# Kernel optimization log

Hardware: AMD Instinct MI355X
Metric: run time of the kernel (lower is better)

## Reference

```python
import jax, jax.numpy as jnp
import numpy as np

EPS = 1e-5
SLOPE = 0.01  # LeakyReLU default negative_slope
D_STATE = 16


def leaky(x):
    return jnp.where(x >= 0, x, SLOPE * x)


def instance_norm(x):
    # InstanceNorm3d(affine=False): normalize per (n, c) over spatial dims
    m = x.mean(axis=(2, 3, 4), keepdims=True)
    v = x.var(axis=(2, 3, 4), keepdims=True)
    return (x - m) * jax.lax.rsqrt(v + EPS)


def conv3d(x, w, b, groups=1, pad=0):
    y = jax.lax.conv_general_dilated(
        x, w, (1, 1, 1), [(pad, pad)] * 3,
        dimension_numbers=('NCDHW', 'OIDHW', 'NCDHW'),
        feature_group_count=groups)
    return y + b[None, :, None, None, None]


def conv_transpose2(x, w, b):
    # ConvTranspose3d(k=2, s=2): non-overlapping, so it is a pure einsum+interleave
    # x: [n,c,d,h,w], w: [c,o,2,2,2] (torch layout)
    y = jnp.einsum('ncdhw,coijk->nodihjwk', x, w)
    n, o, d, _, h, _, ww, _ = y.shape
    return y.reshape(n, o, 2 * d, 2 * h, 2 * ww) + b[None, :, None, None, None]


def selective_scan(u, dt, A, B, C, D):
    # u, dt: [b,l,d]; A: [d,n]; B, C: [b,l,n]; D: [d]
    dA = jnp.exp(dt[..., None] * A)                              # [b,l,d,n]
    dBu = dt[..., None] * B[:, :, None, :] * u[..., None]        # [b,l,d,n]

    def step(h, inp):
        dA_t, dBu_t, C_t = inp
        h = dA_t * h + dBu_t                                     # [b,d,n]
        y = jnp.einsum('bdn,bn->bd', h, C_t)
        return h, y

    h0 = jnp.zeros((u.shape[0],) + A.shape, u.dtype)
    _, ys = jax.lax.scan(
        step, h0,
        (dA.transpose(1, 0, 2, 3), dBu.transpose(1, 0, 2, 3), C.transpose(1, 0, 2)))
    return ys.transpose(1, 0, 2) + u * D                         # [b,l,d]


def mamba_block(x, in_proj_w, conv1d_w, conv1d_b, x_proj_w,
                dt_proj_w, dt_proj_b, A_log, D_param, out_proj_w):
    # x: [b,l,c]
    dt_rank = dt_proj_w.shape[1]
    xz = x @ in_proj_w.T                                         # [b,l,2*d_inner]
    xi, z = jnp.split(xz, 2, axis=-1)
    # causal depthwise conv1d over sequence (torch pads d_conv-1 both sides, keeps [:L])
    xi_c = xi.transpose(0, 2, 1)                                 # [b,d_inner,l]
    xi_c = jax.lax.conv_general_dilated(
        xi_c, conv1d_w, (1,), [(conv1d_w.shape[-1] - 1, 0)],
        dimension_numbers=('NCH', 'OIH', 'NCH'),
        feature_group_count=xi_c.shape[1])
    xi = jax.nn.silu(xi_c + conv1d_b[None, :, None]).transpose(0, 2, 1)  # [b,l,d_inner]
    x_dbl = xi @ x_proj_w.T
    dt, B, C = jnp.split(x_dbl, [dt_rank, dt_rank + D_STATE], axis=-1)
    dt = jax.nn.softplus(dt @ dt_proj_w.T + dt_proj_b)
    A = -jnp.exp(A_log)
    y = selective_scan(xi, dt, A, B, C, D_param)
    y = y * jax.nn.silu(z)
    return y @ out_proj_w.T


def layer_norm(x, w, b):
    m = x.mean(-1, keepdims=True)
    v = x.var(-1, keepdims=True)
    return (x - m) * jax.lax.rsqrt(v + EPS) * w + b


def up_forward(x1, x2, up_w, up_b, dc1_w, dc1_b, dc2_w, dc2_b, dc3_w, dc3_b,
               ln_w, ln_b, in_proj_w, conv1d_w, conv1d_b, x_proj_w,
               dt_proj_w, dt_proj_b, A_log, D_param, out_proj_w):
    x1 = conv_transpose2(x1, up_w, up_b)
    dZ = x2.shape[2] - x1.shape[2]
    dY = x2.shape[3] - x1.shape[3]
    dX = x2.shape[4] - x1.shape[4]
    x1 = jnp.pad(x1, ((0, 0), (0, 0),
                      (dZ // 2, dZ - dZ // 2),
                      (dY // 2, dY - dY // 2),
                      (dX // 2, dX - dX // 2)))
    x = jnp.concatenate([x2, x1], axis=1)
    # DoubleConv (residual=False since in_channels != out_channels)
    x = leaky(instance_norm(conv3d(x, dc1_w, dc1_b)))
    x = leaky(instance_norm(conv3d(x, dc2_w, dc2_b, groups=8, pad=1)))
    x = leaky(instance_norm(conv3d(x, dc3_w, dc3_b)))
    # MambaLayer over flattened spatial tokens
    b, c, d, h, w = x.shape
    t = x.transpose(0, 2, 3, 4, 1).reshape(b, d * h * w, c)
    t = layer_norm(t, ln_w, ln_b)
    t = mamba_block(t, in_proj_w, conv1d_w, conv1d_b, x_proj_w,
                    dt_proj_w, dt_proj_b, A_log, D_param, out_proj_w)
    return t.reshape(b, d, h, w, c).transpose(0, 4, 1, 2, 3)


def setup_inputs() -> dict:
    key = jax.random.key(0)
    ks = jax.random.split(key, 20)
    c_out = 32      # out_channels / d_model
    d_inner = 64    # expand * d_model
    dt_rank = 2     # ceil(32/16)
    s = 0.02
    return {
        'x1': jax.random.normal(ks[0], (2, 32, 8, 16, 16), jnp.float32),
        'x2': jax.random.normal(ks[1], (2, 32, 16, 32, 32), jnp.float32),
        'up_w': jax.random.normal(ks[2], (32, 32, 2, 2, 2), jnp.float32) * s,
        'up_b': jnp.zeros((32,), jnp.float32),
        'dc1_w': jax.random.normal(ks[3], (32, 64, 1, 1, 1), jnp.float32) * s,
        'dc1_b': jnp.zeros((32,), jnp.float32),
        'dc2_w': jax.random.normal(ks[4], (32, 4, 3, 3, 3), jnp.float32) * s,
        'dc2_b': jnp.zeros((32,), jnp.float32),
        'dc3_w': jax.random.normal(ks[5], (32, 32, 1, 1, 1), jnp.float32) * s,
        'dc3_b': jnp.zeros((32,), jnp.float32),
        'ln_w': jnp.ones((c_out,), jnp.float32),
        'ln_b': jnp.zeros((c_out,), jnp.float32),
        'in_proj_w': jax.random.normal(ks[6], (2 * d_inner, c_out), jnp.float32) * s,
        'conv1d_w': jax.random.normal(ks[7], (d_inner, 1, 4), jnp.float32) * s,
        'conv1d_b': jnp.zeros((d_inner,), jnp.float32),
        'x_proj_w': jax.random.normal(ks[8], (dt_rank + 2 * D_STATE, d_inner), jnp.float32) * s,
        'dt_proj_w': jax.random.normal(ks[9], (d_inner, dt_rank), jnp.float32) * s,
        'dt_proj_b': jnp.full((d_inner,), -4.0, jnp.float32),
        'A_log': jnp.log(jnp.tile(jnp.arange(1.0, D_STATE + 1.0, dtype=jnp.float32), (d_inner, 1))),
        'D_param': jnp.ones((d_inner,), jnp.float32),
        'out_proj_w': jax.random.normal(ks[10], (c_out, d_inner), jnp.float32) * s,
    }


def reference(x1, x2, up_w, up_b, dc1_w, dc1_b, dc2_w, dc2_b, dc3_w, dc3_b,
              ln_w, ln_b, in_proj_w, conv1d_w, conv1d_b, x_proj_w,
              dt_proj_w, dt_proj_b, A_log, D_param, out_proj_w):
    return up_forward(x1, x2, up_w, up_b, dc1_w, dc1_b, dc2_w, dc2_b, dc3_w, dc3_b,
                      ln_w, ln_b, in_proj_w, conv1d_w, conv1d_b, x_proj_w,
                      dt_proj_w, dt_proj_b, A_log, D_param, out_proj_w)
```

## Files before the change

kernel.cpp:

```cpp
#include <hip/hip_runtime.h>

#define TPB 256
#define S_TOT 16384
#define NCHUNK 512
#define CLEN 32
#define EPS 1e-5f
#define SLOPE 0.01f

__device__ __forceinline__ float leakyf(float v){ return v > 0.f ? v : SLOPE * v; }
__device__ __forceinline__ float siluf(float v){ return v / (1.f + __expf(-v)); }

__global__ __launch_bounds__(TPB) void k_upc1(
    const float* __restrict__ x1, const float* __restrict__ x2,
    const float* __restrict__ upw, const float* __restrict__ upb,
    const float* __restrict__ w1, const float* __restrict__ b1,
    float* __restrict__ c1, float* st1p) {
  __shared__ float wq[8192];
  __shared__ float sup[64*33];
  __shared__ float red[4][8][2];
  int t = threadIdx.x, bid = blockIdx.x;
  int sb = bid & 255, n = bid >> 8;
  int p = t & 63, os = t >> 6;
  int s = sb*64 + p;
  for (int i = t; i < 8192; i += TPB) wq[i] = upw[i];
  __syncthreads();
  int z = s >> 10, y = (s >> 5) & 31, x = s & 31;
  int tap = ((z & 1)*2 + (y & 1))*2 + (x & 1);
  int xb = n*65536 + (z >> 1)*256 + (y >> 1)*16 + (x >> 1);
  float xv[32];
  #pragma unroll
  for (int c = 0; c < 32; c++) xv[c] = x1[xb + c*2048];
  float up[8];
  #pragma unroll
  for (int j = 0; j < 8; j++) up[j] = upb[os*8 + j];
  #pragma unroll
  for (int c = 0; c < 32; c++) {
    #pragma unroll
    for (int j = 0; j < 8; j++)
      up[j] += xv[c] * wq[c*256 + (os*8 + j)*8 + tap];
  }
  #pragma unroll
  for (int j = 0; j < 8; j++) sup[p*33 + os*8 + j] = up[j];
  __syncthreads();
  int c0 = os*8;
  float acc[8];
  #pragma unroll
  for (int j = 0; j < 8; j++) acc[j] = b1[c0 + j];
  const float* px2 = x2 + n*32*S_TOT + s;
  #pragma unroll
  for (int i = 0; i < 32; i++) {
    float v = px2[i*S_TOT];
    #pragma unroll
    for (int j = 0; j < 8; j++) acc[j] += v * w1[(c0 + j)*64 + i];
  }
  #pragma unroll
  for (int o = 0; o < 32; o++) {
    float v = sup[p*33 + o];
    #pragma unroll
    for (int j = 0; j < 8; j++) acc[j] += v * w1[(c0 + j)*64 + 32 + o];
  }
  #pragma unroll
  for (int j = 0; j < 8; j++)
    c1[(n*32 + c0 + j)*S_TOT + s] = acc[j];
  int wv = t >> 6;
  #pragma unroll
  for (int j = 0; j < 8; j++) {
    float sm = acc[j], sq = acc[j]*acc[j];
    #pragma unroll
    for (int o = 32; o > 0; o >>= 1) { sm += __shfl_down(sm, o); sq += __shfl_down(sq, o); }
    if ((t & 63) == 0) { red[wv][j][0] = sm; red[wv][j][1] = sq; }
  }
  __syncthreads();
  if (t < 64) {
    int w2 = t >> 4, j = (t >> 1) & 7, m = t & 1;
    st1p[((n*32 + w2*8 + j)*2 + m)*256 + sb] = red[w2][j][m];
  }
}

__global__ __launch_bounds__(TPB) void k_conv2(
    const float* __restrict__ c1, const float* __restrict__ w,
    const float* __restrict__ bias, const float* st1p,
    float* __restrict__ c2, float* st2p) {
  __shared__ float ws[432];
  __shared__ float tile[4080];
  __shared__ float smom[4][2];
  __shared__ float mrs[4][2];
  __shared__ float red[4][4][2];
  int bid = blockIdx.x, t = threadIdx.x;
  int sb = bid & 63, g = (bid >> 6) & 7, n = bid >> 9;
  int s0 = sb << 8;
  int z = s0 >> 10, y0 = (s0 >> 5) & 31;
  for (int i = t; i < 432; i += TPB) ws[i] = w[g*432 + i];
  {
    int pp = t >> 5, l = t & 31;
    if (pp < 8) {
      int j = pp & 3, m = pp >> 2;
      const float* sp = st1p + ((n*32 + g*4 + j)*2 + m)*256;
      float v = 0.f;
      #pragma unroll
      for (int k = 0; k < 8; k++) v += sp[l + 32*k];
      v += __shfl_down(v, 16); v += __shfl_down(v, 8); v += __shfl_down(v, 4);
      v += __shfl_down(v, 2);  v += __shfl_down(v, 1);
      if (l == 0) smom[j][m] = v;
    }
  }
  __syncthreads();
  if (t < 4) {
    float m = smom[t][0] * (1.f/S_TOT);
    mrs[t][0] = m; mrs[t][1] = rsqrtf(smom[t][1]*(1.f/S_TOT) - m*m + EPS);
  }
  __syncthreads();
  const float* cbase = c1 + (n*32 + g*4)*S_TOT;
  for (int i = t; i < 4080; i += TPB) {
    int ic = i / 1020, r = i - ic*1020;
    int zo = r / 340, r2 = r - zo*340;
    int yo = r2 / 34, xo = r2 - yo*34;
    int zz = z + zo - 1, yy = y0 + yo - 1, xx = xo - 1;
    float v = 0.f;
    if (zz >= 0 && zz < 16 && yy >= 0 && yy < 32 && xx >= 0 && xx < 32)
      v = leakyf((cbase[ic*S_TOT + zz*1024 + yy*32 + xx] - mrs[ic][0]) * mrs[ic][1]);
    tile[i] = v;
  }
  __syncthreads();
  int ty = t >> 5, x = t & 31;
  int s = s0 + t;
  float acc[4];
  #pragma unroll
  for (int oc = 0; oc < 4; oc++) acc[oc] = bias[g*4 + oc];
  #pragma unroll
  for (int ic = 0; ic < 4; ic++) {
    #pragma unroll
    for (int dz = 0; dz < 3; dz++) {
      #pragma unroll
      for (int dy = 0; dy < 3; dy++) {
        const float* tr = tile + ((ic*3 + dz)*10 + ty + dy)*34 + x;
        float p0 = tr[0], p1 = tr[1], p2 = tr[2];
        int wb = ic*27 + dz*9 + dy*3;
        #pragma unroll
        for (int oc = 0; oc < 4; oc++) {
          const float* wo = &ws[oc*108 + wb];
          acc[oc] += p0*wo[0] + p1*wo[1] + p2*wo[2];
        }
      }
    }
  }
  float sm[4], sq[4];
  #pragma unroll
  for (int oc = 0; oc < 4; oc++) {
    c2[(n*32 + g*4 + oc)*S_TOT + s] = acc[oc];
    sm[oc] = acc[oc]; sq[oc] = acc[oc]*acc[oc];
  }
  #pragma unroll
  for (int o = 32; o > 0; o >>= 1) {
    #pragma unroll
    for (int oc = 0; oc < 4; oc++) {
      sm[oc] += __shfl_down(sm[oc], o);
      sq[oc] += __shfl_down(sq[oc], o);
    }
  }
  int lane = t & 63, wv = t >> 6;
  if (lane == 0) {
    #pragma unroll
    for (int oc = 0; oc < 4; oc++) { red[wv][oc][0] = sm[oc]; red[wv][oc][1] = sq[oc]; }
  }
  __syncthreads();
  if (t < 8) {
    int oc = t & 3, m = t >> 2;
    float a = red[0][oc][m] + red[1][oc][m] + red[2][oc][m] + red[3][oc][m];
    st2p[((n*32 + g*4 + oc)*2 + m)*64 + sb] = a;
  }
}

__global__ __launch_bounds__(TPB) void k_conv3(
    const float* __restrict__ c2, const float* __restrict__ w,
    const float* __restrict__ bias, const float* st2p,
    float* __restrict__ c3, float* st3p) {
  __shared__ float ws[256];
  __shared__ float ssum[32][2];
  __shared__ float mrs[32][2];
  __shared__ float red[4][8][2];
  int t = threadIdx.x;
  int idx = blockIdx.x * TPB + t;
  int s = idx & 16383;
  int n = (idx >> 14) & 1;
  int q = idx >> 15;
  int sb = blockIdx.x & 63;
  int c0 = q*8;
  if (t < 256) ws[t] = w[c0*32 + t];
  if (t < 64) {
    int c = t >> 1, m = t & 1;
    const float* sp = st2p + ((n*32 + c)*2 + m)*64;
    float v = 0.f;
    #pragma unroll
    for (int k = 0; k < 64; k++) v += sp[k];
    ssum[c][m] = v;
  }
  __syncthreads();
  if (t < 32) {
    float m = ssum[t][0] * (1.f/S_TOT);
    mrs[t][0] = m; mrs[t][1] = rsqrtf(ssum[t][1]*(1.f/S_TOT) - m*m + EPS);
  }
  __syncthreads();
  const float* pin = c2 + n*32*S_TOT + s;
  float acc[8];
  #pragma unroll
  for (int j = 0; j < 8; j++) acc[j] = bias[c0 + j];
  #pragma unroll
  for (int i = 0; i < 32; i++) {
    float v = leakyf((pin[i*S_TOT] - mrs[i][0]) * mrs[i][1]);
    #pragma unroll
    for (int j = 0; j < 8; j++) acc[j] += v * ws[j*32 + i];
  }
  #pragma unroll
  for (int j = 0; j < 8; j++)
    c3[(n*32 + c0 + j)*S_TOT + s] = acc[j];
  int wv = t >> 6;
  #pragma unroll
  for (int j = 0; j < 8; j++) {
    float sm = acc[j], sq = acc[j]*acc[j];
    #pragma unroll
    for (int o = 32; o > 0; o >>= 1) { sm += __shfl_down(sm, o); sq += __shfl_down(sq, o); }
    if ((t & 63) == 0) { red[wv][j][0] = sm; red[wv][j][1] = sq; }
  }
  __syncthreads();
  if (t < 16) {
    int j = t >> 1, m = t & 1;
    float a = red[0][j][m] + red[1][j][m] + red[2][j][m] + red[3][j][m];
    st3p[((n*32 + c0 + j)*2 + m)*64 + sb] = a;
  }
}

__global__ __launch_bounds__(TPB) void k_token(
    const float* __restrict__ c3, const float* st3p,
    const float* __restrict__ lnw, const float* __restrict__ lnb,
    const float* __restrict__ ipw, const float* __restrict__ c1w,
    const float* __restrict__ c1b, const float* __restrict__ xpw,
    const float* __restrict__ dtw, const float* __restrict__ dtbi,
    float* __restrict__ zb, float* __restrict__ u, float* __restrict__ dt,
    float* __restrict__ Bb, float* __restrict__ Cc) {
  __shared__ float un[4224];
  __shared__ float xpf[3264];
  __shared__ float sxi[2240];
  __shared__ float lnwb[64];
  __shared__ float mrs[64];
  __shared__ float ssum[64];
  float* Wraw = un;
  float* tk   = un;
  float* mv   = un + 1280;
  float* su2  = un;
  float* xd   = un + 2176;

  int t = threadIdx.x, bid = blockIdx.x;
  int tok0 = bid * 32;
  int n = tok0 >> 14, s0 = tok0 & 16383;

  if (t < 64) {
    int c = t >> 1, m = t & 1;
    const float* sp = st3p + ((n*32 + c)*2 + m)*64;
    float v = 0.f;
    #pragma unroll
    for (int k = 0; k < 64; k++) v += sp[k];
    ssum[c*2 + m] = v;
  }
  for (int i = t; i < 4096; i += TPB) {
    int f = i >> 5, c = i & 31;
    Wraw[f*33 + c] = ipw[i];
  }
  for (int i = t; i < 3264; i += TPB) {
    int f = i / 68, dd = i - f*68;
    xpf[i] = (f < 34 && dd < 64) ? xpw[f*64 + dd] : 0.f;
  }
  if (t < 32) { lnwb[t] = lnw[t]; lnwb[32 + t] = lnb[t]; }
  __syncthreads();
  if (t < 32) {
    float m = ssum[t*2] * (1.f/S_TOT);
    mrs[t*2] = m; mrs[t*2 + 1] = rsqrtf(ssum[t*2 + 1]*(1.f/S_TOT) - m*m + EPS);
  }
  int fr = t & 127, half = t >> 7;
  float wreg[32];
  float S1 = 0.f, S2 = 0.f;
  #pragma unroll
  for (int c = 0; c < 32; c++) {
    float wa = Wraw[fr*33 + c];
    wreg[c] = wa * lnwb[c];
    S1 += wreg[c];
    S2 += wa * lnwb[32 + c];
  }
  __syncthreads();
  for (int i = t; i < 1120; i += TPB) {
    int c = i / 35, lt = i - c*35;
    int sg = s0 - 3 + lt;
    int sgc = sg < 0 ? 0 : sg;
    float raw = c3[(n*32 + c)*S_TOT + sgc];
    tk[lt*36 + c] = leakyf((raw - mrs[c*2]) * mrs[c*2 + 1]);
  }
  __syncthreads();
  if (t < 35) {
    float mean = 0.f;
    #pragma unroll
    for (int c = 0; c < 32; c++) mean += tk[t*36 + c];
    mean *= (1.f/32.f);
    float var = 0.f;
    #pragma unroll
    for (int c = 0; c < 32; c++) { float d2 = tk[t*36 + c] - mean; var += d2*d2; }
    mv[t*2] = mean; mv[t*2 + 1] = rsqrtf(var*(1.f/32.f) + EPS);
  }
  __syncthreads();
  for (int lt = half; lt < 35; lt += 2) {
    float acc = 0.f;
    #pragma unroll
    for (int c4 = 0; c4 < 8; c4++) {
      float4 tq = *(const float4*)(tk + lt*36 + 4*c4);
      acc += wreg[4*c4]*tq.x + wreg[4*c4+1]*tq.y + wreg[4*c4+2]*tq.z + wreg[4*c4+3]*tq.w;
    }
    float mean = mv[lt*2], rst = mv[lt*2 + 1];
    float r = rst*(acc - mean*S1) + S2;
    int sg = s0 - 3 + lt;
    if (fr < 64) {
      sxi[lt*64 + fr] = (sg < 0) ? 0.f : r;
    } else if (lt >= 3) {
      zb[(tok0 + lt - 3)*64 + (fr - 64)] = r;
    }
  }
  __syncthreads();
  int ch = t & 63;
  {
    float cw0 = c1w[ch*4], cw1 = c1w[ch*4+1], cw2 = c1w[ch*4+2], cw3 = c1w[ch*4+3];
    float cb = c1b[ch];
    #pragma unroll
    for (int r = 0; r < 8; r++) {
      int lt = (t >> 6) + 4*r;
      float acc = cb + sxi[lt*64 + ch]*cw0 + sxi[(lt+1)*64 + ch]*cw1
                     + sxi[(lt+2)*64 + ch]*cw2 + sxi[(lt+3)*64 + ch]*cw3;
      float uv = siluf(acc);
      u[(tok0 + lt)*64 + ch] = uv;
      su2[lt*68 + ch] = uv;
    }
  }
  __syncthreads();
  #pragma unroll
  for (int pass = 0; pass < 2; pass++) {
    int lt = (t >> 4) + pass*16;
    int f0 = (t & 15)*3;
    const float* sr = su2 + lt*68;
    const float* xr0 = xpf + f0*68;
    const float* xr1 = xpf + (f0+1)*68;
    const float* xr2 = xpf + (f0+2)*68;
    float a0 = 0.f, a1 = 0.f, a2 = 0.f;
    #pragma unroll
    for (int c4 = 0; c4 < 16; c4++) {
      float4 uq = *(const float4*)(sr + 4*c4);
      float4 q0 = *(const float4*)(xr0 + 4*c4);
      float4 q1 = *(const float4*)(xr1 + 4*c4);
      float4 q2 = *(const float4*)(xr2 + 4*c4);
      a0 += uq.x*q0.x + uq.y*q0.y + uq.z*q0.z + uq.w*q0.w;
      a1 += uq.x*q1.x + uq.y*q1.y + uq.z*q1.z + uq.w*q1.w;
      a2 += uq.x*q2.x + uq.y*q2.y + uq.z*q2.z + uq.w*q2.w;
    }
    if (f0     < 34) xd[lt*34 + f0]     = a0;
    if (f0 + 1 < 34) xd[lt*34 + f0 + 1] = a1;
    if (f0 + 2 < 34) xd[lt*34 + f0 + 2] = a2;
  }
  __syncthreads();
  {
    float dw0 = dtw[ch*2], dw1 = dtw[ch*2+1], db = dtbi[ch];
    #pragma unroll
    for (int r = 0; r < 8; r++) {
      int lt = (t >> 6) + 4*r;
      int token = tok0 + lt;
      float dv = xd[lt*34]*dw0 + xd[lt*34 + 1]*dw1 + db;
      dt[token*64 + ch] = fmaxf(dv, 0.f) + log1pf(__expf(-fabsf(dv)));
      if (ch < 16)      Bb[token*16 + ch]      = xd[lt*34 + 2 + ch];
      else if (ch < 32) Cc[token*16 + ch - 16] = xd[lt*34 + 2 + ch];
    }
  }
}


__global__ __launch_bounds__(TPB) void k_scan1(
    const float* __restrict__ dt, const float* __restrict__ u,
    const float* __restrict__ Bb, const float* __restrict__ Alog,
    float* __restrict__ cA, float* __restrict__ cX) {
  __shared__ __align__(16) float sdt[1024], su[1024], sB[256];
  int bid = blockIdx.x, t = threadIdx.x;
  int chunk = bid & (NCHUNK-1), b = bid >> 9;
  int q = t & 3, d = t >> 2;
  float Ar[4];
  #pragma unroll
  for (int j = 0; j < 4; j++) Ar[j] = -__expf(Alog[d*16 + 4*q + j]);
  float h[4] = {0.f,0.f,0.f,0.f};
  float sdts = 0.f;
  int tg0 = b*S_TOT + chunk*CLEN;
  for (int tile = 0; tile < 2; tile++) {
    int base = tg0 + tile*16;
    {
      int i = t*4;
      *(float4*)(sdt + i) = *(const float4*)(dt + base*64 + i);
      *(float4*)(su  + i) = *(const float4*)(u  + base*64 + i);
    }
    sB[t] = Bb[base*16 + t];
    __syncthreads();
    #pragma unroll
    for (int tt = 0; tt < 16; tt++) {
      float dtv = sdt[tt*64 + d], uv = su[tt*64 + d];
      sdts += dtv;
      float du = dtv * uv;
      float4 Bq = *(const float4*)(sB + tt*16 + q*4);
      h[0] = __expf(Ar[0]*dtv)*h[0] + Bq.x*du;
      h[1] = __expf(Ar[1]*dtv)*h[1] + Bq.y*du;
      h[2] = __expf(Ar[2]*dtv)*h[2] + Bq.z*du;
      h[3] = __expf(Ar[3]*dtv)*h[3] + Bq.w*du;
    }
    __syncthreads();
  }
  #pragma unroll
  for (int j = 0; j < 4; j++) {
    int idx = (((b*64 + d)*16 + 4*q + j)*NCHUNK) + chunk;
    cA[idx] = __expf(Ar[j]*sdts);
    cX[idx] = h[j];
  }
}

__global__ __launch_bounds__(TPB) void k_scan2(
    const float* __restrict__ cA, float* __restrict__ cX) {
  int t = threadIdx.x;
  int w = blockIdx.x*4 + (t >> 6);
  int lane = t & 63;
  int b = w >> 10, d = (w >> 4) & 63, nn = w & 15;
  int base = ((b*64 + d)*16 + nn)*NCHUNK;
  float a[8], x[8];
  *(float4*)(a)     = *(const float4*)(cA + base + lane*8);
  *(float4*)(a + 4) = *(const float4*)(cA + base + lane*8 + 4);
  *(float4*)(x)     = *(const float4*)(cX + base + lane*8);
  *(float4*)(x + 4) = *(const float4*)(cX + base + lane*8 + 4);
  float A = 1.f, X = 0.f;
  #pragma unroll
  for (int k = 0; k < 8; k++) { X = X*a[k] + x[k]; A *= a[k]; }
  #pragma unroll
  for (int off = 1; off < 64; off <<= 1) {
    float Ap = __shfl_up(A, off);
    float Xp = __shfl_up(X, off);
    if (lane >= off) { X = A*Xp + X; A = A*Ap; }
  }
  float Xe = __shfl_up(X, 1);
  if (lane == 0) Xe = 0.f;
  float r = Xe;
  float o[8];
  #pragma unroll
  for (int k = 0; k < 8; k++) { o[k] = r; r = a[k]*r + x[k]; }
  *(float4*)(cX + base + lane*8)     = *(float4*)(o);
  *(float4*)(cX + base + lane*8 + 4) = *(float4*)(o + 4);
}

__global__ __launch_bounds__(TPB) void k_scan3(
    const float* __restrict__ dt, const float* __restrict__ u,
    const float* __restrict__ Bb, const float* __restrict__ Cc,
    const float* __restrict__ Alog, const float* __restrict__ Dp,
    const float* __restrict__ zb, const float* __restrict__ cX,
    const float* __restrict__ opw, float* __restrict__ out) {
  __shared__ __align__(16) float sdt[1024], su[1024], sB[256], sC[256];
  __shared__ float gt[32*65];
  int bid = blockIdx.x, t = threadIdx.x;
  int chunk = bid & (NCHUNK-1), b = bid >> 9;
  int q = t & 3, d = t >> 2;
  float Ar[4];
  #pragma unroll
  for (int j = 0; j < 4; j++) Ar[j] = -__expf(Alog[d*16 + 4*q + j]);
  float h[4];
  #pragma unroll
  for (int j = 0; j < 4; j++)
    h[j] = cX[(((b*64 + d)*16 + 4*q + j)*NCHUNK) + chunk];
  float Dv = Dp[d];
  int tg0 = b*S_TOT + chunk*CLEN;
  for (int tile = 0; tile < 2; tile++) {
    int base = tg0 + tile*16;
    {
      int i = t*4;
      *(float4*)(sdt + i) = *(const float4*)(dt + base*64 + i);
      *(float4*)(su  + i) = *(const float4*)(u  + base*64 + i);
    }
    for (int i = t; i < 1024; i += TPB)
      gt[(tile*16 + (i >> 6))*65 + (i & 63)] = zb[base*64 + i];
    sB[t] = Bb[base*16 + t];
    sC[t] = Cc[base*16 + t];
    __syncthreads();
    #pragma unroll
    for (int tt = 0; tt < 16; tt++) {
      float dtv = sdt[tt*64 + d], uv = su[tt*64 + d];
      float du = dtv * uv;
      float4 Bq = *(const float4*)(sB + tt*16 + q*4);
      float4 Cq = *(const float4*)(sC + tt*16 + q*4);
      h[0] = __expf(Ar[0]*dtv)*h[0] + Bq.x*du;
      h[1] = __expf(Ar[1]*dtv)*h[1] + Bq.y*du;
      h[2] = __expf(Ar[2]*dtv)*h[2] + Bq.z*du;
      h[3] = __expf(Ar[3]*dtv)*h[3] + Bq.w*du;
      float yp = h[0]*Cq.x + h[1]*Cq.y + h[2]*Cq.z + h[3]*Cq.w;
      yp += __shfl_xor(yp, 1);
      yp += __shfl_xor(yp, 2);
      if (q == 0) {
        float zv = gt[(tile*16 + tt)*65 + d];
        gt[(tile*16 + tt)*65 + d] = (yp + uv*Dv) * siluf(zv);
      }
    }
    __syncthreads();
  }
  {
    int sl = t & 31, cb = t >> 5;
    float acc[4] = {0.f,0.f,0.f,0.f};
    const float* wp = opw + cb*4*64;
    #pragma unroll
    for (int dd = 0; dd < 64; dd++) {
      float v = gt[sl*65 + dd];
      #pragma unroll
      for (int j = 0; j < 4; j++) acc[j] += v * wp[j*64 + dd];
    }
    #pragma unroll
    for (int j = 0; j < 4; j++)
      out[(b*32 + cb*4 + j)*S_TOT + chunk*CLEN + sl] = acc[j];
  }
}

extern "C" void kernel_launch(void* const* d_in, const int* in_sizes, int n_in,
                              void* d_out, int out_size, void* d_ws, size_t ws_size,
                              hipStream_t stream) {
  const float* x1    = (const float*)d_in[0];
  const float* x2    = (const float*)d_in[1];
  const float* upw   = (const float*)d_in[2];
  const float* upb   = (const float*)d_in[3];
  const float* dc1w  = (const float*)d_in[4];
  const float* dc1b  = (const float*)d_in[5];
  const float* dc2w  = (const float*)d_in[6];
  const float* dc2b  = (const float*)d_in[7];
  const float* dc3w  = (const float*)d_in[8];
  const float* dc3b  = (const float*)d_in[9];
  const float* lnw   = (const float*)d_in[10];
  const float* lnb   = (const float*)d_in[11];
  const float* ipw   = (const float*)d_in[12];
  const float* c1w   = (const float*)d_in[13];
  const float* c1b   = (const float*)d_in[14];
  const float* xpw   = (const float*)d_in[15];
  const float* dtw   = (const float*)d_in[16];
  const float* dtbi  = (const float*)d_in[17];
  const float* Alog  = (const float*)d_in[18];
  const float* Dp    = (const float*)d_in[19];
  const float* opw   = (const float*)d_in[20];
  float* out = (float*)d_out;

  float* ws = (float*)d_ws;
  float* st1p  = ws + 0;
  float* st2p  = ws + 32768;
  float* st3p  = ws + 40960;
  float* c1    = ws + 49152;
  float* c2    = ws + 1097728;
  float* c3    = ws + 2146304;
  float* zb    = ws + 3194880;
  float* ub    = ws + 5292032;
  float* dtb   = ws + 7389184;
  float* Bb    = ws + 9486336;
  float* Cc    = ws + 10010624;
  float* cA    = ws + 10534912;
  float* cX    = ws + 11583488;

  k_upc1 <<<512,  TPB, 0, stream>>>(x1, x2, upw, upb, dc1w, dc1b, c1, st1p);
  k_conv2<<<1024, TPB, 0, stream>>>(c1, dc2w, dc2b, st1p, c2, st2p);
  k_conv3<<<512,  TPB, 0, stream>>>(c2, dc3w, dc3b, st2p, c3, st3p);
  k_token<<<1024, TPB, 0, stream>>>(c3, st3p, lnw, lnb, ipw, c1w, c1b, xpw,
                                    dtw, dtbi, zb, ub, dtb, Bb, Cc);
  k_scan1<<<1024, TPB, 0, stream>>>(dtb, ub, Bb, Alog, cA, cX);
  k_scan2<<<512,  TPB, 0, stream>>>(cA, cX);
  k_scan3<<<1024, TPB, 0, stream>>>(dtb, ub, Bb, Cc, Alog, Dp, zb, cX, opw, out);
}
```

Baseline: 236.5 us.

## Fuse chunk-local scan pass into token projection kernel

Removes the separate k_scan1 launch by computing each chunk's local selective-scan state and decay product at the end of k_token, reading dt, u and B straight from shared memory instead of reloading them from global memory. Each k_token block already covers exactly one 32-token chunk, so the chunk mapping carries over. It also adds a min-blocks-per-CU hint of 4 to k_token's launch bounds, which may limit registers. The extra work lengthens k_token and reuses shared buffers (sxi, su2, xd), so correctness depends on those regions still holding valid data.

```diff
diff --git a/kernel.cpp b/kernel.cpp
--- a/kernel.cpp
+++ b/kernel.cpp
@@ -230,14 +230,16 @@
   }
 }
 
-__global__ __launch_bounds__(TPB) void k_token(
+__global__ __launch_bounds__(TPB, 4) void k_token(
     const float* __restrict__ c3, const float* st3p,
     const float* __restrict__ lnw, const float* __restrict__ lnb,
     const float* __restrict__ ipw, const float* __restrict__ c1w,
     const float* __restrict__ c1b, const float* __restrict__ xpw,
     const float* __restrict__ dtw, const float* __restrict__ dtbi,
+    const float* __restrict__ Alog,
     float* __restrict__ zb, float* __restrict__ u, float* __restrict__ dt,
-    float* __restrict__ Bb, float* __restrict__ Cc) {
+    float* __restrict__ Bb, float* __restrict__ Cc,
+    float* __restrict__ cA, float* __restrict__ cX) {
   __shared__ float un[4224];
   __shared__ float xpf[3264];
   __shared__ float sxi[2240];
@@ -249,10 +251,12 @@
   float* mv   = un + 1280;
   float* su2  = un;
   float* xd   = un + 2176;
+  float* sdt2 = sxi;
 
   int t = threadIdx.x, bid = blockIdx.x;
   int tok0 = bid * 32;
   int n = tok0 >> 14, s0 = tok0 & 16383;
+  int chunk = bid & (NCHUNK - 1);
 
   if (t < 64) {
     int c = t >> 1, m = t & 1;
@@ -369,57 +373,41 @@
       int lt = (t >> 6) + 4*r;
       int token = tok0 + lt;
       float dv = xd[lt*34]*dw0 + xd[lt*34 + 1]*dw1 + db;
-      dt[token*64 + ch] = fmaxf(dv, 0.f) + log1pf(__expf(-fabsf(dv)));
+      float sp = fmaxf(dv, 0.f) + log1pf(__expf(-fabsf(dv)));
+      dt[token*64 + ch] = sp;
+      sdt2[lt*64 + ch] = sp;
       if (ch < 16)      Bb[token*16 + ch]      = xd[lt*34 + 2 + ch];
       else if (ch < 32) Cc[token*16 + ch - 16] = xd[lt*34 + 2 + ch];
     }
   }
-}
-
-
-__global__ __launch_bounds__(TPB) void k_scan1(
-    const float* __restrict__ dt, const float* __restrict__ u,
-    const float* __restrict__ Bb, const float* __restrict__ Alog,
-    float* __restrict__ cA, float* __restrict__ cX) {
-  __shared__ __align__(16) float sdt[1024], su[1024], sB[256];
-  int bid = blockIdx.x, t = threadIdx.x;
-  int chunk = bid & (NCHUNK-1), b = bid >> 9;
-  int q = t & 3, d = t >> 2;
-  float Ar[4];
-  #pragma unroll
-  for (int j = 0; j < 4; j++) Ar[j] = -__expf(Alog[d*16 + 4*q + j]);
-  float h[4] = {0.f,0.f,0.f,0.f};
-  float sdts = 0.f;
-  int tg0 = b*S_TOT + chunk*CLEN;
-  for (int tile = 0; tile < 2; tile++) {
-    int base = tg0 + tile*16;
-    {
-      int i = t*4;
-      *(float4*)(sdt + i) = *(const float4*)(dt + base*64 + i);
-      *(float4*)(su  + i) = *(const float4*)(u  + base*64 + i);
-    }
-    sB[t] = Bb[base*16 + t];
-    __syncthreads();
-    #pragma unroll
-    for (int tt = 0; tt < 16; tt++) {
-      float dtv = sdt[tt*64 + d], uv = su[tt*64 + d];
+  __syncthreads();
+  {
+    int q = t & 3, d = t >> 2;
+    float Ar0 = -__expf(Alog[d*16 + 4*q]);
+    float Ar1 = -__expf(Alog[d*16 + 4*q + 1]);
+    float Ar2 = -__expf(Alog[d*16 + 4*q + 2]);
+    float Ar3 = -__expf(Alog[d*16 + 4*q + 3]);
+    float h0 = 0.f, h1 = 0.f, h2 = 0.f, h3 = 0.f, sdts = 0.f;
+    #pragma unroll 4
+    for (int tt = 0; tt < CLEN; tt++) {
+      float dtv = sdt2[tt*64 + d], uv = su2[tt*68 + d];
       sdts += dtv;
       float du = dtv * uv;
-      float4 Bq = *(const float4*)(sB + tt*16 + q*4);
-      h[0] = __expf(Ar[0]*dtv)*h[0] + Bq.x*du;
-      h[1] = __expf(Ar[1]*dtv)*h[1] + Bq.y*du;
-      h[2] = __expf(Ar[2]*dtv)*h[2] + Bq.z*du;
-      h[3] = __expf(Ar[3]*dtv)*h[3] + Bq.w*du;
-    }
-    __syncthreads();
-  }
-  #pragma unroll
-  for (int j = 0; j < 4; j++) {
-    int idx = (((b*64 + d)*16 + 4*q + j)*NCHUNK) + chunk;
-    cA[idx] = __expf(Ar[j]*sdts);
-    cX[idx] = h[j];
-  }
-}
+      const float* bp = xd + tt*34 + 2 + 4*q;
+      float B0 = bp[0], B1 = bp[1], B2 = bp[2], B3 = bp[3];
+      h0 = __expf(Ar0*dtv)*h0 + B0*du;
+      h1 = __expf(Ar1*dtv)*h1 + B1*du;
+      h2 = __expf(Ar2*dtv)*h2 + B2*du;
+      h3 = __expf(Ar3*dtv)*h3 + B3*du;
+    }
+    int base = (((n*64 + d)*16 + 4*q)*NCHUNK) + chunk;
+    cA[base]            = __expf(Ar0*sdts); cX[base]            = h0;
+    cA[base + NCHUNK]   = __expf(Ar1*sdts); cX[base + NCHUNK]   = h1;
+    cA[base + 2*NCHUNK] = __expf(Ar2*sdts); cX[base + 2*NCHUNK] = h2;
+    cA[base + 3*NCHUNK] = __expf(Ar3*sdts); cX[base + 3*NCHUNK] = h3;
+  }
+}
+
 
 __global__ __launch_bounds__(TPB) void k_scan2(
     const float* __restrict__ cA, float* __restrict__ cX) {
@@ -565,8 +553,7 @@
   k_conv2<<<1024, TPB, 0, stream>>>(c1, dc2w, dc2b, st1p, c2, st2p);
   k_conv3<<<512,  TPB, 0, stream>>>(c2, dc3w, dc3b, st2p, c3, st3p);
   k_token<<<1024, TPB, 0, stream>>>(c3, st3p, lnw, lnb, ipw, c1w, c1b, xpw,
-                                    dtw, dtbi, zb, ub, dtb, Bb, Cc);
-  k_scan1<<<1024, TPB, 0, stream>>>(dtb, ub, Bb, Alog, cA, cX);
+                                    dtw, dtbi, Alog, zb, ub, dtb, Bb, Cc, cA, cX);
   k_scan2<<<512,  TPB, 0, stream>>>(cA, cX);
   k_scan3<<<1024, TPB, 0, stream>>>(dtb, ub, Bb, Cc, Alog, Dp, zb, cX, opw, out);
 }
```

Measured after the change: 284.3 us. +20.2%, slower.
